# Performance work log

Measured on AMD Instinct MI355X. Metric: run time of the kernel, lower is better.

## Reference

```python
import jax, jax.numpy as jnp
import numpy as np

B, NPG = 128, 128          # graphs, nodes per graph
N = B * NPG                # total nodes
K = 16                     # kNN neighbors within cutoff
D = 256                    # embedding_depth
H, DH = 4, 32              # heads = num_layers, head dim = (D//2)//H
L = 4                      # num graph convolutions
NR = 50                    # num_radial
CUTOFF = 2.0
OUT = 3 + 100              # 3 + max_ntypes


def setup_inputs() -> dict:
    rng = np.random.default_rng(0)
    pos = rng.standard_normal((N, 3)).astype(np.float32)
    nbrs = np.zeros((N, K), np.int32)
    mask = np.zeros((N, K), np.float32)
    for g in range(B):  # per-graph kNN with radial cutoff (setup only, numpy)
        p = pos[g * NPG:(g + 1) * NPG]
        d2 = ((p[:, None, :] - p[None, :, :]) ** 2).sum(-1)
        np.fill_diagonal(d2, np.inf)
        idx = np.argsort(d2, axis=1)[:, :K]
        dk = np.sqrt(np.take_along_axis(d2, idx, 1))
        nbrs[g * NPG:(g + 1) * NPG] = idx + g * NPG
        mask[g * NPG:(g + 1) * NPG] = (dk <= CUTOFF).astype(np.float32)
    batch_idx = np.repeat(np.arange(B, dtype=np.int32), NPG)

    key = jax.random.key(0)
    ks = jax.random.split(key, 12)
    s = 0.02
    return {
        'encoding': jax.random.normal(ks[0], (B, D), jnp.float32),
        'pos': jnp.asarray(pos),
        'batch_idx': jnp.asarray(batch_idx),
        'neighbors': jnp.asarray(nbrs),
        'nbr_mask': jnp.asarray(mask),
        'W_in': jax.random.normal(ks[1], (D + 3, D), jnp.float32) * s,
        'b_in': jnp.zeros((D,), jnp.float32),
        'Wq': jax.random.normal(ks[2], (L, D, H * DH), jnp.float32) * s,
        'Wk': jax.random.normal(ks[3], (L, D, H * DH), jnp.float32) * s,
        'Wv': jax.random.normal(ks[4], (L, D, H * DH), jnp.float32) * s,
        'We': jax.random.normal(ks[5], (L, NR, H * DH), jnp.float32) * s,
        'Wo': jax.random.normal(ks[6], (L, H * DH, D), jnp.float32) * s,
        'bo': jnp.zeros((L, D), jnp.float32),
        'Wfc': jax.random.normal(ks[7], (L, D, D), jnp.float32) * s,
        'bfc': jnp.zeros((L, D), jnp.float32),
        'ln_g': jnp.ones((L, D), jnp.float32),
        'ln_b': jnp.zeros((L, D), jnp.float32),
        'W_out': jax.random.normal(ks[8], (D, OUT), jnp.float32) * s,
        'b_out': jnp.zeros((OUT,), jnp.float32),
    }


def reference(encoding, pos, batch_idx, neighbors, nbr_mask,
              W_in, b_in, Wq, Wk, Wv, We, Wo, bo, Wfc, bfc,
              ln_g, ln_b, W_out, b_out):
    # x = encoding.repeat_interleave(graph_sizes); x[:, 0] = 1
    x = encoding[batch_idx]                      # [N, D]
    x = x.at[:, 0].set(1.0)
    h = jnp.concatenate([x, pos], axis=-1) @ W_in + b_in   # concat pos, embed

    # gaussian radial basis of neighbor distances
    dvec = pos[neighbors] - pos[:, None, :]      # [N, K, 3]
    d = jnp.sqrt((dvec ** 2).sum(-1) + 1e-12)    # [N, K]
    centers = jnp.linspace(0.0, CUTOFF, NR)
    width = centers[1] - centers[0]
    rbf = jnp.exp(-0.5 * ((d[..., None] - centers) / width) ** 2)  # [N, K, NR]

    scale = 1.0 / jnp.sqrt(jnp.float32(DH))
    m = nbr_mask[..., None]                      # [N, K, 1]
    for l in range(L):                           # TransformerConv layers
        q = (h @ Wq[l]).reshape(N, H, DH)
        k = (h @ Wk[l]).reshape(N, H, DH)
        v = (h @ Wv[l]).reshape(N, H, DH)
        e = (rbf @ We[l]).reshape(N, K, H, DH)   # edge embedding
        kj = k[neighbors] + e                    # [N, K, H, DH]
        vj = v[neighbors] + e
        logits = jnp.einsum('nhd,nkhd->nkh', q, kj) * scale
        logits = jnp.where(m > 0, logits, -1e9)
        a = jax.nn.softmax(logits, axis=1) * m   # masked attention over K
        msg = jnp.einsum('nkh,nkhd->nhd', a, vj).reshape(N, H * DH)
        h = h + msg @ Wo[l] + bo[l]              # residual update
        mu = h.mean(-1, keepdims=True)
        var = h.var(-1, keepdims=True)
        h = ln_g[l] * (h - mu) / jnp.sqrt(var + 1e-5) + ln_b[l]
        h = jax.nn.gelu(h @ Wfc[l] + bfc[l])     # nodewise fc (1 layer)

    return h @ W_out + b_out                     # [N, 3 + max_ntypes]
```

## Files before the change

kernel.cpp:

```cpp
#include <hip/hip_runtime.h>
#include <hip/hip_bf16.h>
#include <math.h>

#define N_PTS 16384
#define NLAYER 4

typedef __attribute__((ext_vector_type(8))) short bfrag;
typedef __attribute__((ext_vector_type(4))) float f32x4;
typedef unsigned short ushort_t;
typedef unsigned int uint_t;

__device__ __forceinline__ ushort_t f2b(float f) {
  __hip_bfloat16 h = __float2bfloat16(f);
  return *reinterpret_cast<const ushort_t*>(&h);
}
__device__ __forceinline__ float b2f(ushort_t u) {
  union { uint_t i; float f; } c; c.i = ((uint_t)u) << 16; return c.f;
}
__device__ __forceinline__ float blo(uint_t u) {
  union { uint_t i; float f; } c; c.i = u << 16; return c.f;
}
__device__ __forceinline__ float bhi(uint_t u) {
  union { uint_t i; float f; } c; c.i = u & 0xffff0000u; return c.f;
}

#define MFMA16(a, b, c) __builtin_amdgcn_mfma_f32_16x16x32_bf16((a), (b), (c), 0, 0, 0)

__global__ __launch_bounds__(256) void base_kernel(
    const float* __restrict__ enc, const float* __restrict__ W_in,
    const float* __restrict__ b_in, float* __restrict__ base)
{
  int b = blockIdx.x, j = threadIdx.x;
  __shared__ float se[256];
  se[j] = enc[b * 256 + j];
  __syncthreads();
  float acc = b_in[j] + W_in[j];
  for (int i = 1; i < 256; ++i) acc += se[i] * W_in[i * 256 + j];
  base[b * 256 + j] = acc;
}

__global__ __launch_bounds__(256) void embed_kernel(
    const float* __restrict__ base, const int* __restrict__ batch_idx,
    const float* __restrict__ pos, const float* __restrict__ W_in,
    ushort_t* __restrict__ h_bf, ushort_t* __restrict__ hbP)
{
  int n = blockIdx.x, j = threadIdx.x;
  int b = batch_idx[n];
  float px = pos[n * 3 + 0], py = pos[n * 3 + 1], pz = pos[n * 3 + 2];
  float v = base[b * 256 + j]
      + px * W_in[256 * 256 + j] + py * W_in[257 * 256 + j] + pz * W_in[258 * 256 + j];
  ushort_t u = f2b(v);
  h_bf[(size_t)n * 256 + j] = u;
  int rt = n >> 4, ct = j >> 4;
  int lane = ((n & 15) >> 2) * 16 + (j & 15);
  hbP[(((size_t)rt * 16 + ct) * 64 + lane) * 4 + (n & 3)] = u;
}

__global__ __launch_bounds__(256) void prep_qkv(
    const float* __restrict__ Wq, const float* __restrict__ Wk,
    const float* __restrict__ Wv, const float* __restrict__ We,
    ushort_t* __restrict__ out)
{
  int idx = blockIdx.x * 256 + threadIdx.x;
  int l = idx / (640 * 256);
  int rem = idx - l * (640 * 256);
  int c = rem >> 8, k = rem & 255;
  float v = 0.f;
  if (c < 128) v = Wq[((size_t)l * 256 + k) * 128 + c];
  else if (c < 328) {
    int p = c - 128, hq = p / 50, r = p - hq * 50;
    const float* wq = &Wq[((size_t)l * 256 + k) * 128 + hq * 32];
    const float* we = &We[((size_t)l * 50 + r) * 128 + hq * 32];
#pragma unroll
    for (int d = 0; d < 32; ++d) v += wq[d] * we[d];
  } else if (c < 456) v = Wk[((size_t)l * 256 + k) * 128 + (c - 328)];
  else if (c < 584) v = Wv[((size_t)l * 256 + k) * 128 + (c - 456)];
  size_t pos = (size_t)l * 163840
      + (((c >> 4) * 8 + (k >> 5)) * 64 + ((k >> 3) & 3) * 16 + (c & 15)) * 8 + (k & 7);
  out[pos] = f2b(v);
}

__global__ __launch_bounds__(256) void prep_bcat(
    const float* __restrict__ We, const float* __restrict__ Wo, ushort_t* __restrict__ out)
{
  int idx = blockIdx.x * 256 + threadIdx.x;
  if (idx >= 4 * 256 * 352) return;
  int l = idx / (256 * 352);
  int rem = idx - l * (256 * 352);
  int c = rem / 352, k = rem - c * 352;
  float v = 0.f;
  if (k < 128) v = Wo[((size_t)l * 128 + k) * 256 + c];
  else if (k < 328) {
    int p = k - 128, hq = p / 50, r = p - hq * 50;
    const float* we = &We[((size_t)l * 50 + r) * 128 + hq * 32];
    const float* wo = &Wo[((size_t)l * 128 + hq * 32) * 256 + c];
#pragma unroll
    for (int d = 0; d < 32; ++d) v += we[d] * wo[(size_t)d * 256];
  }
  size_t pos = (size_t)l * 90112
      + (((k >> 5) * 16 + (c >> 4)) * 64 + ((k >> 3) & 3) * 16 + (c & 15)) * 8 + (k & 7);
  out[pos] = f2b(v);
}

__global__ __launch_bounds__(256) void prep_wfc(
    const float* __restrict__ Wfc, ushort_t* __restrict__ out)
{
  int idx = blockIdx.x * 256 + threadIdx.x;
  int l = idx >> 16, rem = idx & 65535;
  int c = rem >> 8, k = rem & 255;
  float v = Wfc[((size_t)l * 256 + k) * 256 + c];
  size_t pos = (size_t)l * 65536
      + (((k >> 5) * 16 + (c >> 4)) * 64 + ((k >> 3) & 3) * 16 + (c & 15)) * 8 + (k & 7);
  out[pos] = f2b(v);
}

__global__ __launch_bounds__(256) void prep_wout(
    const float* __restrict__ W_out, ushort_t* __restrict__ out)
{
  int idx = blockIdx.x * 256 + threadIdx.x;
  int c = idx >> 8, k = idx & 255;
  float v = (c < 103) ? W_out[(size_t)k * 103 + c] : 0.f;
  size_t pos = (((c >> 4) * 8 + (k >> 5)) * 64 + ((k >> 3) & 3) * 16 + (c & 15)) * 8 + (k & 7);
  out[pos] = f2b(v);
}

template<int MODE>
__global__ __launch_bounds__(128) void fused_layer(
    const ushort_t* __restrict__ Amsg,
    const ushort_t* __restrict__ BcP,
    const float* __restrict__ bo,
    ushort_t* __restrict__ hbP,
    const float* __restrict__ lg, const float* __restrict__ lb,
    const ushort_t* __restrict__ WfP,
    const float* __restrict__ bfc,
    const ushort_t* __restrict__ W3P,
    const float* __restrict__ b3,
    const ushort_t* __restrict__ h_bf,
    ushort_t* __restrict__ qext_b, ushort_t* __restrict__ kvb,
    float* __restrict__ outF)
{
  __shared__ __align__(16) ushort_t tb[16 * 264];
  __shared__ float pS[2][16], pSS[2][16];

  const int tid = threadIdx.x;
  const int lane = tid & 63, wv = tid >> 6;
  const int l15 = lane & 15, l4 = lane >> 4;
  const int rt = blockIdx.x;
  const int r0 = rt * 16;

  if constexpr (MODE != 2) {
    const int cb = wv * 8;

    bfrag aA[11];
#pragma unroll
    for (int ks = 0; ks < 11; ++ks)
      aA[ks] = *(const bfrag*)(Amsg + (size_t)(r0 + l15) * 352 + ks * 32 + l4 * 8);

    f32x4 acc[8];
#pragma unroll
    for (int j = 0; j < 8; ++j) acc[j] = (f32x4){0.f, 0.f, 0.f, 0.f};
#pragma unroll
    for (int ks = 0; ks < 11; ++ks) {
#pragma unroll
      for (int j = 0; j < 8; ++j) {
        bfrag b = *(const bfrag*)(BcP + (((size_t)ks * 16 + cb + j) * 64 + lane) * 8);
        acc[j] = MFMA16(aA[ks], b, acc[j]);
      }
    }

    float s0 = 0.f, s1 = 0.f, s2 = 0.f, s3 = 0.f;
    float q0 = 0.f, q1 = 0.f, q2 = 0.f, q3 = 0.f;
#pragma unroll
    for (int j = 0; j < 8; ++j) {
      const int c = (cb + j) * 16 + l15;
      const float boc = bo[c];
      uint2 hv = *(const uint2*)(hbP + (((size_t)rt * 16 + cb + j) * 64 + lane) * 4);
      const ushort_t* hu = (const ushort_t*)&hv;
      float x0 = acc[j][0] + boc + b2f(hu[0]);
      float x1 = acc[j][1] + boc + b2f(hu[1]);
      float x2 = acc[j][2] + boc + b2f(hu[2]);
      float x3 = acc[j][3] + boc + b2f(hu[3]);
      acc[j][0] = x0; acc[j][1] = x1; acc[j][2] = x2; acc[j][3] = x3;
      s0 += x0; q0 += x0 * x0; s1 += x1; q1 += x1 * x1;
      s2 += x2; q2 += x2 * x2; s3 += x3; q3 += x3 * x3;
    }
#pragma unroll
    for (int off = 1; off < 16; off <<= 1) {
      s0 += __shfl_xor(s0, off, 64); q0 += __shfl_xor(q0, off, 64);
      s1 += __shfl_xor(s1, off, 64); q1 += __shfl_xor(q1, off, 64);
      s2 += __shfl_xor(s2, off, 64); q2 += __shfl_xor(q2, off, 64);
      s3 += __shfl_xor(s3, off, 64); q3 += __shfl_xor(q3, off, 64);
    }
    if (l15 == 0) {
      pS[wv][l4 * 4 + 0] = s0; pSS[wv][l4 * 4 + 0] = q0;
      pS[wv][l4 * 4 + 1] = s1; pSS[wv][l4 * 4 + 1] = q1;
      pS[wv][l4 * 4 + 2] = s2; pSS[wv][l4 * 4 + 2] = q2;
      pS[wv][l4 * 4 + 3] = s3; pSS[wv][l4 * 4 + 3] = q3;
    }
    __syncthreads();
    float mu[4], inv[4];
#pragma unroll
    for (int i = 0; i < 4; ++i) {
      const int r = l4 * 4 + i;
      float S = pS[0][r] + pS[1][r];
      float Q = pSS[0][r] + pSS[1][r];
      float m = S * (1.f / 256.f);
      float var = Q * (1.f / 256.f) - m * m;
      mu[i] = m;
      inv[i] = 1.0f / sqrtf(var + 1e-5f);
    }
#pragma unroll
    for (int j = 0; j < 8; ++j) {
      const int c = (cb + j) * 16 + l15;
      const float g = lg[c], bb = lb[c];
#pragma unroll
      for (int i = 0; i < 4; ++i)
        tb[(l4 * 4 + i) * 264 + c] = f2b(g * (acc[j][i] - mu[i]) * inv[i] + bb);
    }
    __syncthreads();

    bfrag aH[8];
#pragma unroll
    for (int ks = 0; ks < 8; ++ks)
      aH[ks] = *(const bfrag*)(tb + l15 * 264 + ks * 32 + l4 * 8);
    __syncthreads();

#pragma unroll
    for (int j = 0; j < 8; ++j) acc[j] = (f32x4){0.f, 0.f, 0.f, 0.f};
#pragma unroll
    for (int ks = 0; ks < 8; ++ks) {
#pragma unroll
      for (int j = 0; j < 8; ++j) {
        bfrag b = *(const bfrag*)(WfP + (((size_t)ks * 16 + cb + j) * 64 + lane) * 8);
        acc[j] = MFMA16(aH[ks], b, acc[j]);
      }
    }

#pragma unroll
    for (int j = 0; j < 8; ++j) {
      const int c = (cb + j) * 16 + l15;
      const float bfcc = bfc[c];
      ushort_t uo[4];
#pragma unroll
      for (int i = 0; i < 4; ++i) {
        float x = acc[j][i] + bfcc;
        float t = tanhf(0.7978845608028654f * (x + 0.044715f * x * x * x));
        float gl = 0.5f * x * (1.f + t);
        uo[i] = f2b(gl);
        tb[(l4 * 4 + i) * 264 + c] = uo[i];
      }
      *(uint2*)(hbP + (((size_t)rt * 16 + cb + j) * 64 + lane) * 4) = *(const uint2*)uo;
    }
    __syncthreads();
  }

  bfrag aG[8];
  if constexpr (MODE == 2) {
#pragma unroll
    for (int ks = 0; ks < 8; ++ks)
      aG[ks] = *(const bfrag*)(h_bf + (size_t)(r0 + l15) * 256 + ks * 32 + l4 * 8);
  } else {
#pragma unroll
    for (int ks = 0; ks < 8; ++ks)
      aG[ks] = *(const bfrag*)(tb + l15 * 264 + ks * 32 + l4 * 8);
  }

  const int NCT = (MODE == 1) ? 4 : 20;
  const int cg = wv * NCT;
  for (int ch = 0; ch < NCT; ch += 4) {
    f32x4 a3[4];
#pragma unroll
    for (int j = 0; j < 4; ++j) a3[j] = (f32x4){0.f, 0.f, 0.f, 0.f};
#pragma unroll
    for (int ks = 0; ks < 8; ++ks) {
#pragma unroll
      for (int j = 0; j < 4; ++j) {
        const int ct = cg + ch + j;
        bfrag b = *(const bfrag*)(W3P + (((size_t)ct * 8 + ks) * 64 + lane) * 8);
        a3[j] = MFMA16(aG[ks], b, a3[j]);
      }
    }
#pragma unroll
    for (int j = 0; j < 4; ++j) {
      const int c = (cg + ch + j) * 16 + l15;
#pragma unroll
      for (int i = 0; i < 4; ++i) {
        const size_t r = (size_t)(r0 + l4 * 4 + i);
        float v = a3[j][i];
        if constexpr (MODE == 1) {
          if (c < 103) outF[r * 103 + c] = v + b3[c];
        } else {
          if (c < 328) qext_b[r * 352 + c] = f2b(v);
          else if (c < 584) kvb[r * 256 + (c - 328)] = f2b(v);
        }
      }
    }
  }
}

__global__ __launch_bounds__(256) void attn_kernel(
    const ushort_t* __restrict__ qext, const ushort_t* __restrict__ kvb,
    const float* __restrict__ pos, const int* __restrict__ nbrs,
    const float* __restrict__ mask, ushort_t* __restrict__ Amsg)
{
  __shared__ __align__(16) ushort_t sQ[4][128];
  __shared__ __align__(16) float    sQE[4][4][52];
  __shared__ __align__(16) ushort_t sRbf[4][16][52];
  __shared__ float sA[4][64];
  __shared__ float sD[4][16];
  __shared__ float sMk[4][16];
  __shared__ int   sNb[4][16];

  const int tid = threadIdx.x;
  const int bid = blockIdx.x;
  const int lane = tid & 63, w = tid >> 6;
  const int g = (bid & 7) + 8 * ((bid >> 3) & 15);
  const int q4 = bid >> 7;
  const int kk = lane >> 2, hh = lane & 3;

  for (int it = 0; it < 4; ++it) {
    const int n = g * 128 + q4 * 16 + w * 4 + it;
    if (lane < 16) {
      int nb = nbrs[n * 16 + lane];
      sNb[w][lane] = nb;
      sMk[w][lane] = mask[n * 16 + lane];
      float dx = pos[nb * 3 + 0] - pos[n * 3 + 0];
      float dy = pos[nb * 3 + 1] - pos[n * 3 + 1];
      float dz = pos[nb * 3 + 2] - pos[n * 3 + 2];
      sD[w][lane] = sqrtf(dx * dx + dy * dy + dz * dz + 1e-12f);
      sRbf[w][lane][50] = 0; sRbf[w][lane][51] = 0;
      *(uint4*)(&sQ[w][lane * 8]) = *(const uint4*)(qext + (size_t)n * 352 + lane * 8);
    }
    if (lane < 50) {
      uint2 u = *(const uint2*)(qext + (size_t)n * 352 + 128 + lane * 4);
      int p = lane * 4;
#pragma unroll
      for (int e = 0; e < 4; ++e) {
        ushort_t bb = ((const ushort_t*)&u)[e];
        int pp = p + e, h2 = pp / 50, r = pp - h2 * 50;
        sQE[w][h2][r] = b2f(bb);
      }
    }
    if (lane < 8) sQE[w][lane >> 1][50 + (lane & 1)] = 0.f;
    {
      int kk2 = lane & 15;
      float dk = sD[w][kk2];
      int r0 = lane >> 4;
#pragma unroll
      for (int j = 0; j < 13; ++j) {
        int r = r0 + j * 4;
        if (r < 50) {
          float t = (dk - (2.f / 49.f) * (float)r) * 24.5f;
          sRbf[w][kk2][r] = f2b(__expf(-0.5f * t * t));
        }
      }
    }
    const int nb = sNb[w][kk];
    const ushort_t* krow = kvb + (size_t)nb * 256 + hh * 32;
    float qk = 0.f;
#pragma unroll
    for (int c8 = 0; c8 < 4; ++c8) {
      uint4 kv4 = *(const uint4*)(krow + c8 * 8);
      const uint_t* q4p = (const uint_t*)(&sQ[w][hh * 32 + c8 * 8]);
      uint_t qa = q4p[0], qb = q4p[1], qc = q4p[2], qd = q4p[3];
      qk += blo(qa) * blo(kv4.x) + bhi(qa) * bhi(kv4.x)
          + blo(qb) * blo(kv4.y) + bhi(qb) * bhi(kv4.y)
          + blo(qc) * blo(kv4.z) + bhi(qc) * bhi(kv4.z)
          + blo(qd) * blo(kv4.w) + bhi(qd) * bhi(kv4.w);
    }
    float qe = 0.f;
#pragma unroll
    for (int c = 0; c < 13; ++c) {
      float4 qv = *(const float4*)(&sQE[w][hh][c * 4]);
      uint2 rv = *(const uint2*)(&sRbf[w][kk][c * 4]);
      qe += qv.x * blo(rv.x) + qv.y * bhi(rv.x)
          + qv.z * blo(rv.y) + qv.w * bhi(rv.y);
    }
    float lg = 0.17677669529663687f * (qk + qe);
    lg = (sMk[w][kk] > 0.f) ? lg : -1e9f;

    float mx = lg;
#pragma unroll
    for (int off = 4; off < 64; off <<= 1) mx = fmaxf(mx, __shfl_xor(mx, off, 64));
    float ex = __expf(lg - mx);
    float sm = ex;
#pragma unroll
    for (int off = 4; off < 64; off <<= 1) sm += __shfl_xor(sm, off, 64);
    sA[w][kk * 4 + hh] = ex / sm * sMk[w][kk];

    if (lane < 50) {
      float r0 = 0.f, r1 = 0.f, r2 = 0.f, r3 = 0.f;
#pragma unroll
      for (int k2 = 0; k2 < 16; ++k2) {
        float rb = b2f(sRbf[w][k2][lane]);
        r0 += sA[w][k2 * 4 + 0] * rb;
        r1 += sA[w][k2 * 4 + 1] * rb;
        r2 += sA[w][k2 * 4 + 2] * rb;
        r3 += sA[w][k2 * 4 + 3] * rb;
      }
      Amsg[(size_t)n * 352 + 128 + 0 * 50 + lane] = f2b(r0);
      Amsg[(size_t)n * 352 + 128 + 1 * 50 + lane] = f2b(r1);
      Amsg[(size_t)n * 352 + 128 + 2 * 50 + lane] = f2b(r2);
      Amsg[(size_t)n * 352 + 128 + 3 * 50 + lane] = f2b(r3);
    }
    {
      const int h2 = lane >> 4;
      float m0v = 0.f, m1v = 0.f;
#pragma unroll
      for (int k2 = 0; k2 < 16; ++k2) {
        int nb2 = sNb[w][k2];
        uint_t vv = *(const uint_t*)(kvb + (size_t)nb2 * 256 + 128 + lane * 2);
        float a = sA[w][k2 * 4 + h2];
        m0v += a * blo(vv);
        m1v += a * bhi(vv);
      }
      uint_t o = (uint_t)f2b(m0v) | ((uint_t)f2b(m1v) << 16);
      *(uint_t*)(&Amsg[(size_t)n * 352 + lane * 2]) = o;
    }
    if (lane < 24) Amsg[(size_t)n * 352 + 328 + lane] = 0;
  }
}

extern "C" void kernel_launch(void* const* d_in, const int* in_sizes, int n_in,
                              void* d_out, int out_size, void* d_ws, size_t ws_size,
                              hipStream_t stream) {
  const float* enc    = (const float*)d_in[0];
  const float* pos    = (const float*)d_in[1];
  const int*   bidx   = (const int*)  d_in[2];
  const int*   nbrs   = (const int*)  d_in[3];
  const float* mask   = (const float*)d_in[4];
  const float* W_in   = (const float*)d_in[5];
  const float* b_in   = (const float*)d_in[6];
  const float* Wq     = (const float*)d_in[7];
  const float* Wk     = (const float*)d_in[8];
  const float* Wv     = (const float*)d_in[9];
  const float* We     = (const float*)d_in[10];
  const float* Wo     = (const float*)d_in[11];
  const float* bo     = (const float*)d_in[12];
  const float* Wfc    = (const float*)d_in[13];
  const float* bfc    = (const float*)d_in[14];
  const float* ln_g   = (const float*)d_in[15];
  const float* ln_b   = (const float*)d_in[16];
  const float* W_out  = (const float*)d_in[17];
  const float* b_out  = (const float*)d_in[18];
  float* out = (float*)d_out;

  const int N = N_PTS;
  ushort_t* ws = (ushort_t*)d_ws;
  ushort_t* hbP    = ws;
  ushort_t* h_bf   = hbP + (size_t)N * 256;
  ushort_t* qext_b = h_bf + (size_t)N * 256;
  ushort_t* kvb    = qext_b + (size_t)N * 352;
  ushort_t* Amsg   = kvb + (size_t)N * 256;
  float*    base   = (float*)(Amsg + (size_t)N * 352);
  ushort_t* W3P    = (ushort_t*)(base + 128 * 256);
  ushort_t* BcP    = W3P + 4 * 163840;
  ushort_t* WfP    = BcP + 4 * 90112;
  ushort_t* WoP    = WfP + 4 * 65536;

  base_kernel<<<128, 256, 0, stream>>>(enc, W_in, b_in, base);
  embed_kernel<<<N, 256, 0, stream>>>(base, bidx, pos, W_in, h_bf, hbP);
  prep_qkv<<<(4 * 640 * 256) / 256, 256, 0, stream>>>(Wq, Wk, Wv, We, W3P);
  prep_bcat<<<(4 * 256 * 352 + 255) / 256, 256, 0, stream>>>(We, Wo, BcP);
  prep_wfc<<<(4 * 256 * 256) / 256, 256, 0, stream>>>(Wfc, WfP);
  prep_wout<<<(128 * 256) / 256, 256, 0, stream>>>(W_out, WoP);

  fused_layer<2><<<N / 16, 128, 0, stream>>>(
      nullptr, nullptr, nullptr, nullptr, nullptr, nullptr, nullptr, nullptr,
      W3P, nullptr, h_bf, qext_b, kvb, nullptr);

  for (int l = 0; l < NLAYER; ++l) {
    const ushort_t* BcP_l = BcP + (size_t)l * 90112;
    const ushort_t* WfP_l = WfP + (size_t)l * 65536;
    const float* bo_l  = bo  + (size_t)l * 256;
    const float* bfc_l = bfc + (size_t)l * 256;
    const float* lg_l  = ln_g + (size_t)l * 256;
    const float* lb_l  = ln_b + (size_t)l * 256;

    attn_kernel<<<1024, 256, 0, stream>>>(qext_b, kvb, pos, nbrs, mask, Amsg);

    if (l < NLAYER - 1) {
      const ushort_t* W3P_next = W3P + (size_t)(l + 1) * 163840;
      fused_layer<0><<<N / 16, 128, 0, stream>>>(
          Amsg, BcP_l, bo_l, hbP, lg_l, lb_l, WfP_l, bfc_l,
          W3P_next, nullptr, nullptr, qext_b, kvb, nullptr);
    } else {
      fused_layer<1><<<N / 16, 128, 0, stream>>>(
          Amsg, BcP_l, bo_l, hbP, lg_l, lb_l, WfP_l, bfc_l,
          WoP, b_out, nullptr, nullptr, nullptr, out);
    }
  }
}
```

Baseline: 370.7 us.

## Restructure fused layer: 32-row tiles, 4 waves, async LDS weight ring pipeline

The fused layer kernel now processes 32 rows per block with 4 waves instead of 16 rows with 2 waves, so each weight fragment feeds two MFMAs. The A operands are staged in swizzled shared memory. Weight fragments stream through a per-wave 8-slot LDS ring using global_load_lds, with prefetch depth 6 and vmcnt waits. The aim is to halve weight traffic per row and hide global load latency behind MFMA. The cost is more LDS use (about 60KB), which lowers occupancy, plus a serialized per-iteration wait that may limit overlap.

```diff
diff --git a/kernel.cpp b/kernel.cpp
--- a/kernel.cpp
+++ b/kernel.cpp
@@ -24,7 +24,15 @@
   union { uint_t i; float f; } c; c.i = u & 0xffff0000u; return c.f;
 }
 
+__device__ __forceinline__ void gload16(const ushort_t* g, ushort_t* l) {
+  __builtin_amdgcn_global_load_lds(
+      (const __attribute__((address_space(1))) unsigned int*)g,
+      (__attribute__((address_space(3))) unsigned int*)l, 16, 0, 0);
+}
+
 #define MFMA16(a, b, c) __builtin_amdgcn_mfma_f32_16x16x32_bf16((a), (b), (c), 0, 0, 0)
+#define WVM5() asm volatile("s_waitcnt vmcnt(5)" ::: "memory")
+#define WVM0() asm volatile("s_waitcnt vmcnt(0)" ::: "memory")
 
 __global__ __launch_bounds__(256) void base_kernel(
     const float* __restrict__ enc, const float* __restrict__ W_in,
@@ -125,7 +133,7 @@
 }
 
 template<int MODE>
-__global__ __launch_bounds__(128) void fused_layer(
+__global__ __launch_bounds__(256) void fused_layer(
     const ushort_t* __restrict__ Amsg,
     const ushort_t* __restrict__ BcP,
     const float* __restrict__ bo,
@@ -139,162 +147,227 @@
     ushort_t* __restrict__ qext_b, ushort_t* __restrict__ kvb,
     float* __restrict__ outF)
 {
-  __shared__ __align__(16) ushort_t tb[16 * 264];
-  __shared__ float pS[2][16], pSS[2][16];
+  __shared__ __align__(16) ushort_t sA[32 * 384];
+  __shared__ __align__(16) ushort_t sH[32 * 256];
+  __shared__ __align__(16) ushort_t ring[4 * 8 * 512];
+  __shared__ float pS[4][32], pSS[4][32];
 
   const int tid = threadIdx.x;
   const int lane = tid & 63, wv = tid >> 6;
   const int l15 = lane & 15, l4 = lane >> 4;
-  const int rt = blockIdx.x;
-  const int r0 = rt * 16;
+  const int r7 = l15 & 7;
+  const int r0 = blockIdx.x * 32;
+  const int rtg = blockIdx.x * 2;
+  ushort_t* ring_w = ring + wv * (8 * 512);
+  const int loff = lane * 8;
 
   if constexpr (MODE != 2) {
-    const int cb = wv * 8;
-
-    bfrag aA[11];
-#pragma unroll
-    for (int ks = 0; ks < 11; ++ks)
-      aA[ks] = *(const bfrag*)(Amsg + (size_t)(r0 + l15) * 352 + ks * 32 + l4 * 8);
-
-    f32x4 acc[8];
-#pragma unroll
-    for (int j = 0; j < 8; ++j) acc[j] = (f32x4){0.f, 0.f, 0.f, 0.f};
-#pragma unroll
-    for (int ks = 0; ks < 11; ++ks) {
-#pragma unroll
-      for (int j = 0; j < 8; ++j) {
-        bfrag b = *(const bfrag*)(BcP + (((size_t)ks * 16 + cb + j) * 64 + lane) * 8);
-        acc[j] = MFMA16(aA[ks], b, acc[j]);
-      }
-    }
-
-    float s0 = 0.f, s1 = 0.f, s2 = 0.f, s3 = 0.f;
-    float q0 = 0.f, q1 = 0.f, q2 = 0.f, q3 = 0.f;
-#pragma unroll
-    for (int j = 0; j < 8; ++j) {
-      const int c = (cb + j) * 16 + l15;
-      const float boc = bo[c];
-      uint2 hv = *(const uint2*)(hbP + (((size_t)rt * 16 + cb + j) * 64 + lane) * 4);
-      const ushort_t* hu = (const ushort_t*)&hv;
-      float x0 = acc[j][0] + boc + b2f(hu[0]);
-      float x1 = acc[j][1] + boc + b2f(hu[1]);
-      float x2 = acc[j][2] + boc + b2f(hu[2]);
-      float x3 = acc[j][3] + boc + b2f(hu[3]);
-      acc[j][0] = x0; acc[j][1] = x1; acc[j][2] = x2; acc[j][3] = x3;
-      s0 += x0; q0 += x0 * x0; s1 += x1; q1 += x1 * x1;
-      s2 += x2; q2 += x2 * x2; s3 += x3; q3 += x3 * x3;
-    }
-#pragma unroll
-    for (int off = 1; off < 16; off <<= 1) {
-      s0 += __shfl_xor(s0, off, 64); q0 += __shfl_xor(q0, off, 64);
-      s1 += __shfl_xor(s1, off, 64); q1 += __shfl_xor(q1, off, 64);
-      s2 += __shfl_xor(s2, off, 64); q2 += __shfl_xor(q2, off, 64);
-      s3 += __shfl_xor(s3, off, 64); q3 += __shfl_xor(q3, off, 64);
-    }
-    if (l15 == 0) {
-      pS[wv][l4 * 4 + 0] = s0; pSS[wv][l4 * 4 + 0] = q0;
-      pS[wv][l4 * 4 + 1] = s1; pSS[wv][l4 * 4 + 1] = q1;
-      pS[wv][l4 * 4 + 2] = s2; pSS[wv][l4 * 4 + 2] = q2;
-      pS[wv][l4 * 4 + 3] = s3; pSS[wv][l4 * 4 + 3] = q3;
+    for (int i = tid; i < 32 * 48; i += 256) {
+      int r = i / 48, c8 = i - r * 48;
+      uint4 v = (uint4){0, 0, 0, 0};
+      if (c8 < 44) v = *(const uint4*)(Amsg + (size_t)(r0 + r) * 352 + c8 * 8);
+      *(uint4*)(&sA[r * 384 + ((c8 ^ (r & 7)) << 3)]) = v;
     }
     __syncthreads();
-    float mu[4], inv[4];
-#pragma unroll
-    for (int i = 0; i < 4; ++i) {
-      const int r = l4 * 4 + i;
-      float S = pS[0][r] + pS[1][r];
-      float Q = pSS[0][r] + pSS[1][r];
-      float m = S * (1.f / 256.f);
-      float var = Q * (1.f / 256.f) - m * m;
-      mu[i] = m;
-      inv[i] = 1.0f / sqrtf(var + 1e-5f);
-    }
-#pragma unroll
-    for (int j = 0; j < 8; ++j) {
-      const int c = (cb + j) * 16 + l15;
-      const float g = lg[c], bb = lb[c];
-#pragma unroll
-      for (int i = 0; i < 4; ++i)
-        tb[(l4 * 4 + i) * 264 + c] = f2b(g * (acc[j][i] - mu[i]) * inv[i] + bb);
-    }
+
+    const int cb = wv * 4;
+
+    f32x4 acc[2][4];
+#pragma unroll
+    for (int m = 0; m < 2; ++m)
+#pragma unroll
+      for (int j = 0; j < 4; ++j) acc[m][j] = (f32x4){0.f, 0.f, 0.f, 0.f};
+#pragma unroll
+    for (int p = 0; p < 6; ++p) {
+      int blk = (p >> 2) * 16 + cb + (p & 3);
+      gload16(BcP + (size_t)blk * 512 + loff, ring_w + (p & 7) * 512);
+    }
+    {
+      bfrag a0, a1;
+      for (int i = 0; i < 44; ++i) {
+        WVM5();
+        const int ks = i >> 2, j = i & 3;
+        bfrag b = *(const bfrag*)(ring_w + (i & 7) * 512 + loff);
+        if (j == 0) {
+          const int ch = ks * 4 + l4;
+          a0 = *(const bfrag*)(sA + l15 * 384 + ((ch ^ r7) << 3));
+          a1 = *(const bfrag*)(sA + (16 + l15) * 384 + ((ch ^ r7) << 3));
+        }
+        __builtin_amdgcn_s_setprio(1);
+        acc[0][j] = MFMA16(a0, b, acc[0][j]);
+        acc[1][j] = MFMA16(a1, b, acc[1][j]);
+        __builtin_amdgcn_s_setprio(0);
+        int pn = i + 6; if (pn > 43) pn = 43;
+        int blkn = (pn >> 2) * 16 + cb + (pn & 3);
+        gload16(BcP + (size_t)blkn * 512 + loff, ring_w + ((i + 6) & 7) * 512);
+      }
+      WVM0();
+    }
+
+#pragma unroll
+    for (int m = 0; m < 2; ++m)
+#pragma unroll
+      for (int i = 0; i < 4; ++i) {
+        const int rl = m * 16 + l4 * 4 + i;
+        float s = 0.f, q = 0.f;
+#pragma unroll
+        for (int j = 0; j < 4; ++j) {
+          const int c = (cb + j) * 16 + l15;
+          float hv = b2f(hbP[(((size_t)(rtg + m) * 16 + cb + j) * 64 + lane) * 4 + i]);
+          float x = acc[m][j][i] + bo[c] + hv;
+          acc[m][j][i] = x;
+          s += x; q += x * x;
+        }
+#pragma unroll
+        for (int off = 1; off < 16; off <<= 1) {
+          s += __shfl_xor(s, off, 64);
+          q += __shfl_xor(q, off, 64);
+        }
+        if (l15 == 0) { pS[wv][rl] = s; pSS[wv][rl] = q; }
+      }
     __syncthreads();
-
-    bfrag aH[8];
-#pragma unroll
-    for (int ks = 0; ks < 8; ++ks)
-      aH[ks] = *(const bfrag*)(tb + l15 * 264 + ks * 32 + l4 * 8);
+#pragma unroll
+    for (int m = 0; m < 2; ++m)
+#pragma unroll
+      for (int i = 0; i < 4; ++i) {
+        const int rl = m * 16 + l4 * 4 + i;
+        float S = pS[0][rl] + pS[1][rl] + pS[2][rl] + pS[3][rl];
+        float Q = pSS[0][rl] + pSS[1][rl] + pSS[2][rl] + pSS[3][rl];
+        float mu = S * (1.f / 256.f);
+        float var = Q * (1.f / 256.f) - mu * mu;
+        float inv = 1.0f / sqrtf(var + 1e-5f);
+#pragma unroll
+        for (int j = 0; j < 4; ++j) {
+          const int c = (cb + j) * 16 + l15;
+          sH[rl * 256 + ((((c >> 3) ^ (rl & 7)) << 3) | (c & 7))] =
+              f2b(lg[c] * (acc[m][j][i] - mu) * inv + lb[c]);
+        }
+      }
     __syncthreads();
 
 #pragma unroll
-    for (int j = 0; j < 8; ++j) acc[j] = (f32x4){0.f, 0.f, 0.f, 0.f};
-#pragma unroll
-    for (int ks = 0; ks < 8; ++ks) {
-#pragma unroll
-      for (int j = 0; j < 8; ++j) {
-        bfrag b = *(const bfrag*)(WfP + (((size_t)ks * 16 + cb + j) * 64 + lane) * 8);
-        acc[j] = MFMA16(aH[ks], b, acc[j]);
-      }
-    }
-
-#pragma unroll
-    for (int j = 0; j < 8; ++j) {
-      const int c = (cb + j) * 16 + l15;
-      const float bfcc = bfc[c];
-      ushort_t uo[4];
-#pragma unroll
-      for (int i = 0; i < 4; ++i) {
-        float x = acc[j][i] + bfcc;
-        float t = tanhf(0.7978845608028654f * (x + 0.044715f * x * x * x));
-        float gl = 0.5f * x * (1.f + t);
-        uo[i] = f2b(gl);
-        tb[(l4 * 4 + i) * 264 + c] = uo[i];
-      }
-      *(uint2*)(hbP + (((size_t)rt * 16 + cb + j) * 64 + lane) * 4) = *(const uint2*)uo;
+    for (int m = 0; m < 2; ++m)
+#pragma unroll
+      for (int j = 0; j < 4; ++j) acc[m][j] = (f32x4){0.f, 0.f, 0.f, 0.f};
+#pragma unroll
+    for (int p = 0; p < 6; ++p) {
+      int blk = (p >> 2) * 16 + cb + (p & 3);
+      gload16(WfP + (size_t)blk * 512 + loff, ring_w + (p & 7) * 512);
+    }
+    {
+      bfrag a0, a1;
+      for (int i = 0; i < 32; ++i) {
+        WVM5();
+        const int ks = i >> 2, j = i & 3;
+        bfrag b = *(const bfrag*)(ring_w + (i & 7) * 512 + loff);
+        if (j == 0) {
+          const int ch = ks * 4 + l4;
+          a0 = *(const bfrag*)(sH + l15 * 256 + ((ch ^ r7) << 3));
+          a1 = *(const bfrag*)(sH + (16 + l15) * 256 + ((ch ^ r7) << 3));
+        }
+        __builtin_amdgcn_s_setprio(1);
+        acc[0][j] = MFMA16(a0, b, acc[0][j]);
+        acc[1][j] = MFMA16(a1, b, acc[1][j]);
+        __builtin_amdgcn_s_setprio(0);
+        int pn = i + 6; if (pn > 31) pn = 31;
+        int blkn = (pn >> 2) * 16 + cb + (pn & 3);
+        gload16(WfP + (size_t)blkn * 512 + loff, ring_w + ((i + 6) & 7) * 512);
+      }
+      WVM0();
+    }
+
+#pragma unroll
+    for (int m = 0; m < 2; ++m)
+#pragma unroll
+      for (int j = 0; j < 4; ++j) {
+        const int c = (cb + j) * 16 + l15;
+        const float bfcc = bfc[c];
+        ushort_t uo[4];
+#pragma unroll
+        for (int i = 0; i < 4; ++i) {
+          const int rl = m * 16 + l4 * 4 + i;
+          float x = acc[m][j][i] + bfcc;
+          float t = tanhf(0.7978845608028654f * (x + 0.044715f * x * x * x));
+          float gl = 0.5f * x * (1.f + t);
+          uo[i] = f2b(gl);
+          sA[rl * 256 + ((((c >> 3) ^ (rl & 7)) << 3) | (c & 7))] = uo[i];
+        }
+        *(uint2*)(hbP + (((size_t)(rtg + m) * 16 + cb + j) * 64 + lane) * 4) =
+            *(const uint2*)uo;
+      }
+    __syncthreads();
+  } else {
+    for (int i = tid; i < 32 * 32; i += 256) {
+      int r = i >> 5, c8 = i & 31;
+      *(uint4*)(&sA[r * 256 + ((c8 ^ (r & 7)) << 3)]) =
+          *(const uint4*)(h_bf + (size_t)(r0 + r) * 256 + c8 * 8);
     }
     __syncthreads();
   }
 
-  bfrag aG[8];
-  if constexpr (MODE == 2) {
-#pragma unroll
-    for (int ks = 0; ks < 8; ++ks)
-      aG[ks] = *(const bfrag*)(h_bf + (size_t)(r0 + l15) * 256 + ks * 32 + l4 * 8);
-  } else {
-#pragma unroll
-    for (int ks = 0; ks < 8; ++ks)
-      aG[ks] = *(const bfrag*)(tb + l15 * 264 + ks * 32 + l4 * 8);
-  }
-
-  const int NCT = (MODE == 1) ? 4 : 20;
-  const int cg = wv * NCT;
-  for (int ch = 0; ch < NCT; ch += 4) {
-    f32x4 a3[4];
-#pragma unroll
-    for (int j = 0; j < 4; ++j) a3[j] = (f32x4){0.f, 0.f, 0.f, 0.f};
-#pragma unroll
-    for (int ks = 0; ks < 8; ++ks) {
-#pragma unroll
-      for (int j = 0; j < 4; ++j) {
-        const int ct = cg + ch + j;
-        bfrag b = *(const bfrag*)(W3P + (((size_t)ct * 8 + ks) * 64 + lane) * 8);
-        a3[j] = MFMA16(aG[ks], b, a3[j]);
-      }
-    }
-#pragma unroll
-    for (int j = 0; j < 4; ++j) {
-      const int c = (cg + ch + j) * 16 + l15;
-#pragma unroll
-      for (int i = 0; i < 4; ++i) {
-        const size_t r = (size_t)(r0 + l4 * 4 + i);
-        float v = a3[j][i];
-        if constexpr (MODE == 1) {
-          if (c < 103) outF[r * 103 + c] = v + b3[c];
-        } else {
-          if (c < 328) qext_b[r * 352 + c] = f2b(v);
-          else if (c < 584) kvb[r * 256 + (c - 328)] = f2b(v);
-        }
-      }
-    }
+  {
+    constexpr int CTC = (MODE == 1) ? 2 : 5;
+    constexpr int NCH = (MODE == 1) ? 1 : 2;
+    constexpr int NPC = 8 * CTC;
+    constexpr int NI3 = NCH * NPC;
+    const int cg = wv * (CTC * NCH);
+#pragma unroll
+    for (int p = 0; p < 6; ++p) {
+      int ks = p / CTC, j = p - ks * CTC;
+      int blk = (cg + j) * 8 + ks;
+      gload16(W3P + (size_t)blk * 512 + loff, ring_w + (p & 7) * 512);
+    }
+    f32x4 a3[2][CTC];
+    bfrag a0, a1;
+    for (int i = 0; i < NI3; ++i) {
+      const int chunk = i / NPC;
+      const int rr = i - chunk * NPC;
+      const int ks = rr / CTC, j = rr - ks * CTC;
+      if (rr == 0) {
+#pragma unroll
+        for (int m = 0; m < 2; ++m)
+#pragma unroll
+          for (int t = 0; t < CTC; ++t) a3[m][t] = (f32x4){0.f, 0.f, 0.f, 0.f};
+      }
+      WVM5();
+      bfrag b = *(const bfrag*)(ring_w + (i & 7) * 512 + loff);
+      if (j == 0) {
+        const int ch = ks * 4 + l4;
+        a0 = *(const bfrag*)(sA + l15 * 256 + ((ch ^ r7) << 3));
+        a1 = *(const bfrag*)(sA + (16 + l15) * 256 + ((ch ^ r7) << 3));
+      }
+      __builtin_amdgcn_s_setprio(1);
+      a3[0][j] = MFMA16(a0, b, a3[0][j]);
+      a3[1][j] = MFMA16(a1, b, a3[1][j]);
+      __builtin_amdgcn_s_setprio(0);
+      if (rr == NPC - 1) {
+        const int ctb = cg + chunk * CTC;
+#pragma unroll
+        for (int t = 0; t < CTC; ++t) {
+          const int c = (ctb + t) * 16 + l15;
+#pragma unroll
+          for (int m = 0; m < 2; ++m)
+#pragma unroll
+            for (int i2 = 0; i2 < 4; ++i2) {
+              const size_t r = (size_t)(r0 + m * 16 + l4 * 4 + i2);
+              float v = a3[m][t][i2];
+              if constexpr (MODE == 1) {
+                if (c < 103) outF[r * 103 + c] = v + b3[c];
+              } else {
+                if (c < 328) qext_b[r * 352 + c] = f2b(v);
+                else if (c < 584) kvb[r * 256 + (c - 328)] = f2b(v);
+              }
+            }
+        }
+      }
+      int pn = i + 6; if (pn > NI3 - 1) pn = NI3 - 1;
+      const int pch = pn / NPC;
+      const int prr = pn - pch * NPC;
+      const int pks = prr / CTC, pj = prr - pks * CTC;
+      int blkn = (cg + pch * CTC + pj) * 8 + pks;
+      gload16(W3P + (size_t)blkn * 512 + loff, ring_w + ((i + 6) & 7) * 512);
+    }
+    WVM0();
   }
 }
 
@@ -465,7 +538,7 @@
   prep_wfc<<<(4 * 256 * 256) / 256, 256, 0, stream>>>(Wfc, WfP);
   prep_wout<<<(128 * 256) / 256, 256, 0, stream>>>(W_out, WoP);
 
-  fused_layer<2><<<N / 16, 128, 0, stream>>>(
+  fused_layer<2><<<N / 32, 256, 0, stream>>>(
       nullptr, nullptr, nullptr, nullptr, nullptr, nullptr, nullptr, nullptr,
       W3P, nullptr, h_bf, qext_b, kvb, nullptr);
 
@@ -481,11 +554,11 @@
 
     if (l < NLAYER - 1) {
       const ushort_t* W3P_next = W3P + (size_t)(l + 1) * 163840;
-      fused_layer<0><<<N / 16, 128, 0, stream>>>(
+      fused_layer<0><<<N / 32, 256, 0, stream>>>(
           Amsg, BcP_l, bo_l, hbP, lg_l, lb_l, WfP_l, bfc_l,
           W3P_next, nullptr, nullptr, qext_b, kvb, nullptr);
     } else {
-      fused_layer<1><<<N / 16, 128, 0, stream>>>(
+      fused_layer<1><<<N / 32, 256, 0, stream>>>(
           Amsg, BcP_l, bo_l, hbP, lg_l, lb_l, WfP_l, bfc_l,
           WoP, b_out, nullptr, nullptr, nullptr, out);
     }
```

After: 669.9 us. +80.7%, slower.
